# Kernel optimization log

Hardware: AMD Instinct MI355X
Metric: run time of the kernel (lower is better)

The kernel has to match this reference:

```python
import jax, jax.numpy as jnp
import numpy as np

N_NODES = 100000
N_EDGES = 1600000
HIDDEN = 128


def setup_inputs() -> dict:
    key = jax.random.key(0)
    k_x, k_w1, k_w2, k_v, k_i, k_o = jax.random.split(key, 6)
    x = jax.random.normal(k_x, (N_NODES, HIDDEN), dtype=jnp.float32)
    # gate1/gate2 are Linear(hidden,1,bias=False); store their weight rows as vectors
    w1 = jax.random.normal(k_w1, (HIDDEN,), dtype=jnp.float32) * 0.1
    w2 = jax.random.normal(k_w2, (HIDDEN,), dtype=jnp.float32) * 0.1
    adj_vals = jax.random.uniform(k_v, (N_EDGES,), dtype=jnp.float32)
    in_idx = jax.random.randint(k_i, (N_EDGES,), 0, N_NODES, dtype=jnp.int32)
    out_idx = jax.random.randint(k_o, (N_EDGES,), 0, N_NODES, dtype=jnp.int32)
    return {"x": x, "w1": w1, "w2": w2, "adj_vals": adj_vals,
            "in_idx": in_idx, "out_idx": out_idx}


def reference(x, w1, w2, adj_vals, in_idx, out_idx):
    # per-node gate scalars: x1 = gate1(x), x2 = gate2(x)  -> [N]
    x1 = x @ w1
    x2 = x @ w2
    # edge gate: tanh(x1[src] + x2[dst]) * adj_value  (dropout is identity in eval mode)
    m = jnp.tanh(x1[in_idx] + x2[out_idx]) * adj_vals  # [E]
    # sparse.mm(adj_alpha, x): out[i] = sum_{e: row(e)=i} m_e * x[col(e)]
    messages = m[:, None] * x[out_idx]                 # [E, d]
    result = jax.ops.segment_sum(messages, in_idx, num_segments=N_NODES)
    return result
```

## Files before the change

### kernel.cpp

```cpp
#include <hip/hip_runtime.h>

#define N_NODES 100000
#define N_EDGES 1600000
#define HIDDEN  128

#define NPB_SHIFT 9
#define NPB       512
#define NB        ((N_NODES + NPB - 1) / NPB)
#define PART_T    512
#define PART_EPT  16
#define PART_EPB  (PART_T * PART_EPT)
#define PART_B    ((N_EDGES + PART_EPB - 1) / PART_EPB)
#define HIST_EPT  16
#define HIST_EPB  (256 * HIST_EPT)
#define HIST_B    ((N_EDGES + HIST_EPB - 1) / HIST_EPB)
#define GATES_B   ((N_NODES * 32 + 255) / 256)
#define FINE_PE   20

#define SCAN_C 16
#define SCAN_T ((N_NODES + SCAN_C - 1) / SCAN_C)
#define SCAN_THREADS 6400
#define SCAN_B (SCAN_THREADS / 256)

__device__ __forceinline__ ushort f2bf(float f) {
    unsigned int u = __float_as_uint(f);
    u = (u + 0x7FFFu + ((u >> 16) & 1u)) >> 16;
    return (ushort)u;
}

__global__ void fagcn_zero(int* __restrict__ bcnt) {
    const int t = (int)threadIdx.x;
    if (t < NB) bcnt[t] = 0;
}

__global__ void fagcn_gates_hist(const float* __restrict__ x,
                                 const float* __restrict__ w1,
                                 const float* __restrict__ w2,
                                 const int*   __restrict__ in_idx,
                                 float* __restrict__ g1,
                                 float* __restrict__ g2,
                                 int*   __restrict__ bcnt,
                                 ushort* __restrict__ xh,
                                 int write_xh,
                                 int with_hist) {
    __shared__ int cnt[NB];
    if ((int)blockIdx.x < GATES_B) {
        const int tid  = blockIdx.x * 256 + (int)threadIdx.x;
        const int node = tid >> 5;
        const int hl   = (int)(threadIdx.x & 31);
        if (node >= N_NODES) return;

        const float4 xv  = *reinterpret_cast<const float4*>(x  + (size_t)node * HIDDEN + hl * 4);
        const float4 w1v = *reinterpret_cast<const float4*>(w1 + hl * 4);
        const float4 w2v = *reinterpret_cast<const float4*>(w2 + hl * 4);

        if (write_xh) {
            ushort4 h;
            h.x = f2bf(xv.x); h.y = f2bf(xv.y); h.z = f2bf(xv.z); h.w = f2bf(xv.w);
            *reinterpret_cast<ushort4*>(xh + (size_t)node * HIDDEN + hl * 4) = h;
        }

        float s1 = xv.x * w1v.x + xv.y * w1v.y + xv.z * w1v.z + xv.w * w1v.w;
        float s2 = xv.x * w2v.x + xv.y * w2v.y + xv.z * w2v.z + xv.w * w2v.w;

        #pragma unroll
        for (int off = 16; off > 0; off >>= 1) {
            s1 += __shfl_down(s1, off, 32);
            s2 += __shfl_down(s2, off, 32);
        }
        if (hl == 0) { g1[node] = s1; g2[node] = s2; }
    } else if (with_hist) {
        const int tid  = (int)threadIdx.x;
        const int base = ((int)blockIdx.x - GATES_B) * HIST_EPB + tid * HIST_EPT;
        for (int j = tid; j < NB; j += 256) cnt[j] = 0;
        __syncthreads();
        if (base < N_EDGES) {
            #pragma unroll
            for (int i = 0; i < 4; ++i) {
                const int4 v = *reinterpret_cast<const int4*>(in_idx + base + i * 4);
                atomicAdd(&cnt[v.x >> NPB_SHIFT], 1);
                atomicAdd(&cnt[v.y >> NPB_SHIFT], 1);
                atomicAdd(&cnt[v.z >> NPB_SHIFT], 1);
                atomicAdd(&cnt[v.w >> NPB_SHIFT], 1);
            }
        }
        __syncthreads();
        for (int j = tid; j < NB; j += 256)
            if (cnt[j]) atomicAdd(&bcnt[j], cnt[j]);
    }
}

__global__ void fagcn_scanb(const int* __restrict__ bcnt,
                            int* __restrict__ sbase,
                            int* __restrict__ bcur) {
    __shared__ int l[256];
    const int t = (int)threadIdx.x;
    const int c = (t < NB) ? bcnt[t] : 0;
    l[t] = c;
    __syncthreads();
    for (int off = 1; off < 256; off <<= 1) {
        int v = (t >= off) ? l[t - off] : 0;
        __syncthreads();
        l[t] += v;
        __syncthreads();
    }
    if (t < NB) { sbase[t] = l[t] - c; bcur[t] = 0; }
    if (t == NB - 1) sbase[NB] = l[t];
}

__global__ void fagcn_part(const float* __restrict__ adj,
                           const int*   __restrict__ in_idx,
                           const int*   __restrict__ out_idx,
                           const int*   __restrict__ sbase,
                           int*         __restrict__ bcur,
                           int2*        __restrict__ stage) {
    __shared__ int cnt[NB], lbase[NB], lcur[NB];
    const int tid  = (int)threadIdx.x;
    const int base = blockIdx.x * PART_EPB + tid * PART_EPT;

    for (int j = tid; j < NB; j += PART_T) { cnt[j] = 0; lcur[j] = 0; }
    __syncthreads();

    int s[PART_EPT];
    const bool act = (base < N_EDGES);
    if (act) {
        #pragma unroll
        for (int i = 0; i < PART_EPT / 4; ++i) {
            const int4 v = *reinterpret_cast<const int4*>(in_idx + base + i * 4);
            s[4 * i + 0] = v.x; s[4 * i + 1] = v.y;
            s[4 * i + 2] = v.z; s[4 * i + 3] = v.w;
        }
        #pragma unroll
        for (int i = 0; i < PART_EPT; ++i)
            atomicAdd(&cnt[s[i] >> NPB_SHIFT], 1);
    }
    __syncthreads();
    for (int j = tid; j < NB; j += PART_T)
        if (cnt[j] > 0) lbase[j] = sbase[j] + atomicAdd(&bcur[j], cnt[j]);
    __syncthreads();
    if (act) {
        #pragma unroll
        for (int i = 0; i < PART_EPT / 4; ++i) {
            const int4   d4 = *reinterpret_cast<const int4*>(out_idx + base + i * 4);
            const float4 a4 = *reinterpret_cast<const float4*>(adj + base + i * 4);
            const int   dd[4] = {d4.x, d4.y, d4.z, d4.w};
            const float aa[4] = {a4.x, a4.y, a4.z, a4.w};
            #pragma unroll
            for (int k = 0; k < 4; ++k) {
                const int src = s[4 * i + k];
                const int b   = src >> NPB_SHIFT;
                const int pos = lbase[b] + atomicAdd(&lcur[b], 1);
                stage[pos] = make_int2(((src & (NPB - 1)) << 17) | dd[k],
                                       __float_as_int(aa[k]));
            }
        }
    }
}

__global__ void fagcn_fine(const int2* __restrict__ stage,
                           const int*  __restrict__ sbase,
                           const float* __restrict__ g1,
                           const float* __restrict__ g2,
                           int*        __restrict__ offsets,
                           int2*       __restrict__ sedge) {
    __shared__ int cnt[NPB];
    __shared__ int cur[NPB];
    __shared__ float g1s[NPB];
    const int b = (int)blockIdx.x;
    const int t = (int)threadIdx.x;

    const int ebeg = sbase[b];
    const int eend = sbase[b + 1];
    const int node = (b << NPB_SHIFT) + t;

    g1s[t] = (node < N_NODES) ? g1[node] : 0.f;
    cnt[t] = 0;
    __syncthreads();

    int2  pay[FINE_PE];
    float gv[FINE_PE];
    #pragma unroll
    for (int i = 0; i < FINE_PE; ++i) {
        const int e = ebeg + t + i * NPB;
        if (e < eend) {
            pay[i] = stage[e];
            gv[i]  = g2[pay[i].x & 0x1FFFF];
            atomicAdd(&cnt[(unsigned)pay[i].x >> 17], 1);
        }
    }
    __syncthreads();

    const int c = cnt[t];
    for (int off = 1; off < NPB; off <<= 1) {
        int v = (t >= off) ? cnt[t - off] : 0;
        __syncthreads();
        cnt[t] += v;
        __syncthreads();
    }
    const int excl = cnt[t] - c;
    cur[t] = ebeg + excl;
    if (node < N_NODES) offsets[node] = ebeg + excl;
    if (b == (int)gridDim.x - 1 && t == 0) offsets[N_NODES] = N_EDGES;
    __syncthreads();

    #pragma unroll
    for (int i = 0; i < FINE_PE; ++i) {
        const int e = ebeg + t + i * NPB;
        if (e < eend) {
            const int slocal = (unsigned)pay[i].x >> 17;
            const float m = tanhf(g1s[slocal] + gv[i]) * __int_as_float(pay[i].y);
            const int pos = atomicAdd(&cur[slocal], 1);
            sedge[pos] = make_int2(pay[i].x & 0x1FFFF, __float_as_int(m));
        }
    }
}

__device__ __forceinline__ void acc8(float* a, uint4 v, float m) {
    const unsigned int u[4] = {v.x, v.y, v.z, v.w};
    #pragma unroll
    for (int i = 0; i < 4; ++i) {
        const float lo = __uint_as_float(u[i] << 16);
        const float hi = __uint_as_float(u[i] & 0xFFFF0000u);
        a[2 * i]     += m * lo;
        a[2 * i + 1] += m * hi;
    }
}

__global__ void fagcn_gather_bf16(const ushort* __restrict__ xh,
                                  const int*   __restrict__ offsets,
                                  const int2*  __restrict__ sedge,
                                  float*       __restrict__ out,
                                  int node_beg, int node_end) {
    const int wave = node_beg + (int)((blockIdx.x * blockDim.x + threadIdx.x) >> 6);
    const int lane = (int)(threadIdx.x & 63);
    if (wave >= node_end) return;

    const int beg = offsets[wave];
    const int end = offsets[wave + 1];
    const int q   = lane >> 4;
    const int ql  = lane & 15;

    float a[8] = {0.f, 0.f, 0.f, 0.f, 0.f, 0.f, 0.f, 0.f};
    float b[8] = {0.f, 0.f, 0.f, 0.f, 0.f, 0.f, 0.f, 0.f};

    int e = beg + q;
    for (; e + 12 < end; e += 16) {
        const int2 ed0 = sedge[e];
        const int2 ed1 = sedge[e + 4];
        const int2 ed2 = sedge[e + 8];
        const int2 ed3 = sedge[e + 12];
        const uint4 v0 = *reinterpret_cast<const uint4*>(xh + (size_t)ed0.x * HIDDEN + ql * 8);
        const uint4 v1 = *reinterpret_cast<const uint4*>(xh + (size_t)ed1.x * HIDDEN + ql * 8);
        const uint4 v2 = *reinterpret_cast<const uint4*>(xh + (size_t)ed2.x * HIDDEN + ql * 8);
        const uint4 v3 = *reinterpret_cast<const uint4*>(xh + (size_t)ed3.x * HIDDEN + ql * 8);
        acc8(a, v0, __int_as_float(ed0.y));
        acc8(b, v1, __int_as_float(ed1.y));
        acc8(a, v2, __int_as_float(ed2.y));
        acc8(b, v3, __int_as_float(ed3.y));
    }
    for (; e < end; e += 4) {
        const int2 ed = sedge[e];
        const uint4 v = *reinterpret_cast<const uint4*>(xh + (size_t)ed.x * HIDDEN + ql * 8);
        acc8(a, v, __int_as_float(ed.y));
    }

    float r[8];
    #pragma unroll
    for (int i = 0; i < 8; ++i) r[i] = a[i] + b[i];
    #pragma unroll
    for (int i = 0; i < 8; ++i) r[i] += __shfl(r[i], lane ^ 16, 64);
    #pragma unroll
    for (int i = 0; i < 8; ++i) r[i] += __shfl(r[i], lane ^ 32, 64);

    if (lane < 16) {
        float* o = out + (size_t)wave * HIDDEN + ql * 8;
        float4 lo = {r[0], r[1], r[2], r[3]};
        float4 hi = {r[4], r[5], r[6], r[7]};
        *reinterpret_cast<float4*>(o)     = lo;
        *reinterpret_cast<float4*>(o + 4) = hi;
    }
}

__global__ void fagcn_hist(const int* __restrict__ in_idx,
                           int* __restrict__ counts) {
    const int e = blockIdx.x * blockDim.x + threadIdx.x;
    if (e < N_EDGES) atomicAdd(&counts[in_idx[e]], 1);
}

__global__ void fagcn_zero_nodes(int* __restrict__ counts) {
    const int i = blockIdx.x * blockDim.x + threadIdx.x;
    if (i < N_NODES) counts[i] = 0;
}

__global__ void fagcn_scan1(const int* __restrict__ counts,
                            int* __restrict__ tsum) {
    const int t = blockIdx.x * blockDim.x + threadIdx.x;
    if (t >= SCAN_THREADS) return;
    int s = 0;
    if (t < SCAN_T) {
        const int beg = t * SCAN_C;
        const int end = (beg + SCAN_C < N_NODES) ? beg + SCAN_C : N_NODES;
        for (int i = beg; i < end; ++i) s += counts[i];
    }
    tsum[t] = s;
}

__global__ void fagcn_scan2(int* __restrict__ tsum) {
    __shared__ int lsum[1024];
    const int t = (int)threadIdx.x;
    const int C = (SCAN_THREADS + 1023) / 1024;
    const int beg = t * C;
    const int end = (beg + C < SCAN_THREADS) ? beg + C : SCAN_THREADS;
    int s = 0;
    for (int i = beg; i < end; ++i) s += tsum[i];
    lsum[t] = s;
    __syncthreads();
    for (int off = 1; off < 1024; off <<= 1) {
        int v = (t >= off) ? lsum[t - off] : 0;
        __syncthreads();
        lsum[t] += v;
        __syncthreads();
    }
    int prefix = (t == 0) ? 0 : lsum[t - 1];
    for (int i = beg; i < end; ++i) {
        const int v = tsum[i];
        tsum[i] = prefix;
        prefix += v;
    }
}

__global__ void fagcn_scan3(int* counts,
                            const int* __restrict__ tsum,
                            int* __restrict__ offsets) {
    const int t = blockIdx.x * blockDim.x + threadIdx.x;
    if (t >= SCAN_T) return;
    const int beg = t * SCAN_C;
    const int end = (beg + SCAN_C < N_NODES) ? beg + SCAN_C : N_NODES;
    int prefix = tsum[t];
    for (int i = beg; i < end; ++i) {
        const int c = counts[i];
        offsets[i] = prefix;
        prefix += c;
        counts[i] = 0;
    }
    if (t == 0) offsets[N_NODES] = N_EDGES;
}

__global__ void fagcn_bin(const float* __restrict__ adj,
                          const int*   __restrict__ in_idx,
                          const int*   __restrict__ out_idx,
                          const float* __restrict__ g1,
                          const float* __restrict__ g2,
                          const int*   __restrict__ offsets,
                          int*         __restrict__ cursor,
                          int2*        __restrict__ sedge) {
    const int e = blockIdx.x * blockDim.x + threadIdx.x;
    if (e >= N_EDGES) return;
    const int src = in_idx[e];
    const int dst = out_idx[e];
    const float m = tanhf(g1[src] + g2[dst]) * adj[e];
    const int pos = offsets[src] + atomicAdd(&cursor[src], 1);
    sedge[pos] = make_int2(dst, __float_as_int(m));
}

__global__ void fagcn_gather_f32(const float* __restrict__ x,
                                 const int*   __restrict__ offsets,
                                 const int2*  __restrict__ sedge,
                                 float*       __restrict__ out) {
    const int wave = (int)((blockIdx.x * blockDim.x + threadIdx.x) >> 6);
    const int lane = (int)(threadIdx.x & 63);
    if (wave >= N_NODES) return;
    const int beg  = offsets[wave];
    const int end  = offsets[wave + 1];
    const int half = lane >> 5;
    const int hl   = lane & 31;
    float4 a0 = {0.f, 0.f, 0.f, 0.f};
    float4 a1 = {0.f, 0.f, 0.f, 0.f};
    int e = beg + half;
    for (; e + 2 < end; e += 4) {
        const int2 ed0 = sedge[e];
        const int2 ed1 = sedge[e + 2];
        const float m0 = __int_as_float(ed0.y);
        const float m1 = __int_as_float(ed1.y);
        const float4 v0 = *reinterpret_cast<const float4*>(x + (size_t)ed0.x * HIDDEN + hl * 4);
        const float4 v1 = *reinterpret_cast<const float4*>(x + (size_t)ed1.x * HIDDEN + hl * 4);
        a0.x += m0 * v0.x; a0.y += m0 * v0.y; a0.z += m0 * v0.z; a0.w += m0 * v0.w;
        a1.x += m1 * v1.x; a1.y += m1 * v1.y; a1.z += m1 * v1.z; a1.w += m1 * v1.w;
    }
    for (; e < end; e += 2) {
        const int2 ed = sedge[e];
        const float m = __int_as_float(ed.y);
        const float4 v = *reinterpret_cast<const float4*>(x + (size_t)ed.x * HIDDEN + hl * 4);
        a0.x += m * v.x; a0.y += m * v.y; a0.z += m * v.z; a0.w += m * v.w;
    }
    float4 a;
    a.x = a0.x + a1.x; a.y = a0.y + a1.y; a.z = a0.z + a1.z; a.w = a0.w + a1.w;
    a.x += __shfl(a.x, lane ^ 32, 64);
    a.y += __shfl(a.y, lane ^ 32, 64);
    a.z += __shfl(a.z, lane ^ 32, 64);
    a.w += __shfl(a.w, lane ^ 32, 64);
    if (half == 0) {
        *reinterpret_cast<float4*>(out + (size_t)wave * HIDDEN + hl * 4) = a;
    }
}

extern "C" void kernel_launch(void* const* d_in, const int* in_sizes, int n_in,
                              void* d_out, int out_size, void* d_ws, size_t ws_size,
                              hipStream_t stream) {
    const float* x        = (const float*)d_in[0];
    const float* w1       = (const float*)d_in[1];
    const float* w2       = (const float*)d_in[2];
    const float* adj_vals = (const float*)d_in[3];
    const int*   in_idx   = (const int*)d_in[4];
    const int*   out_idx  = (const int*)d_in[5];
    float* out = (float*)d_out;

    ushort* xh      = (ushort*)d_ws;
    int2*   sedge   = (int2*)(xh + (size_t)N_NODES * HIDDEN);
    int2*   stage   = sedge + N_EDGES;
    float*  g1      = (float*)(stage + N_EDGES);
    float*  g2      = g1 + N_NODES;
    int*    offsets = (int*)(g2 + N_NODES);
    int*    cursor  = offsets + N_NODES + 1;
    int*    tsum    = cursor + N_NODES;
    int*    bcnt    = tsum + SCAN_THREADS;
    int*    sbase   = bcnt + NB;
    int*    bcur    = sbase + NB + 1;

    const size_t need_full = (size_t)((char*)(bcur + NB) - (char*)d_ws);
    const size_t need_old  = need_full - (size_t)N_EDGES * 8;
    const int full_path = (ws_size >= need_full);
    const int bf16_ok   = (ws_size >= need_old);

    if (full_path) {
        fagcn_zero<<<1, 256, 0, stream>>>(bcnt);
        fagcn_gates_hist<<<GATES_B + HIST_B, 256, 0, stream>>>(
            x, w1, w2, in_idx, g1, g2, bcnt, xh, 1, 1);
        fagcn_scanb<<<1, 256, 0, stream>>>(bcnt, sbase, bcur);
        fagcn_part<<<PART_B, PART_T, 0, stream>>>(
            adj_vals, in_idx, out_idx, sbase, bcur, stage);
        fagcn_fine<<<NB, NPB, 0, stream>>>(
            stage, sbase, g1, g2, offsets, sedge);
        const int half_nodes = N_NODES / 2;
        fagcn_gather_bf16<<<(half_nodes + 3) / 4, 256, 0, stream>>>(
            xh, offsets, sedge, out, 0, half_nodes);
        fagcn_gather_bf16<<<(N_NODES - half_nodes + 3) / 4, 256, 0, stream>>>(
            xh, offsets, sedge, out, half_nodes, N_NODES);
    } else {
        if (!bf16_ok) sedge = (int2*)d_ws;
        fagcn_gates_hist<<<GATES_B, 256, 0, stream>>>(
            x, w1, w2, in_idx, g1, g2, bcnt, xh, bf16_ok, 0);
        fagcn_zero_nodes<<<(N_NODES + 255) / 256, 256, 0, stream>>>(cursor);
        fagcn_hist<<<(N_EDGES + 255) / 256, 256, 0, stream>>>(in_idx, cursor);
        fagcn_scan1<<<SCAN_B, 256, 0, stream>>>(cursor, tsum);
        fagcn_scan2<<<1, 1024, 0, stream>>>(tsum);
        fagcn_scan3<<<SCAN_B, 256, 0, stream>>>(cursor, tsum, offsets);
        fagcn_bin<<<(N_EDGES + 255) / 256, 256, 0, stream>>>(
            adj_vals, in_idx, out_idx, g1, g2, offsets, cursor, sedge);
        if (bf16_ok) {
            fagcn_gather_bf16<<<(N_NODES + 3) / 4, 256, 0, stream>>>(
                xh, offsets, sedge, out, 0, N_NODES);
        } else {
            fagcn_gather_f32<<<(N_NODES + 3) / 4, 256, 0, stream>>>(
                x, offsets, sedge, out);
        }
    }
}
```

Before: 149.9 us.

## Reuse atomic ranks for scatter, wave-shuffle scan in fine pass, merge gather launches

The partition and fine-bin kernels now keep the return value of the counting atomicAdd as each edge's rank within its bucket. That removes the second pass of shared-memory atomics used to assign write positions. The fine kernel's 512-element block scan, which needed a __syncthreads per step, becomes a wave-level shuffle scan followed by a small per-wave prefix. The two half-size gather launches are merged into one, and the partition kernel moves to 1024 threads with 8 edges each. Output order inside a bucket may differ, which can change floating-point summation order slightly.

After: 144.0 us. -4.0%, faster.

```diff
diff --git a/kernel.cpp b/kernel.cpp
--- a/kernel.cpp
+++ b/kernel.cpp
@@ -7,8 +7,8 @@
 #define NPB_SHIFT 9
 #define NPB       512
 #define NB        ((N_NODES + NPB - 1) / NPB)
-#define PART_T    512
-#define PART_EPT  16
+#define PART_T    1024
+#define PART_EPT  8
 #define PART_EPB  (PART_T * PART_EPT)
 #define PART_B    ((N_EDGES + PART_EPB - 1) / PART_EPB)
 #define HIST_EPT  16
@@ -114,14 +114,14 @@
                            const int*   __restrict__ sbase,
                            int*         __restrict__ bcur,
                            int2*        __restrict__ stage) {
-    __shared__ int cnt[NB], lbase[NB], lcur[NB];
+    __shared__ int cnt[NB], lbase[NB];
     const int tid  = (int)threadIdx.x;
     const int base = blockIdx.x * PART_EPB + tid * PART_EPT;
 
-    for (int j = tid; j < NB; j += PART_T) { cnt[j] = 0; lcur[j] = 0; }
-    __syncthreads();
-
-    int s[PART_EPT];
+    for (int j = tid; j < NB; j += PART_T) cnt[j] = 0;
+    __syncthreads();
+
+    int s[PART_EPT], rank[PART_EPT];
     const bool act = (base < N_EDGES);
     if (act) {
         #pragma unroll
@@ -132,7 +132,7 @@
         }
         #pragma unroll
         for (int i = 0; i < PART_EPT; ++i)
-            atomicAdd(&cnt[s[i] >> NPB_SHIFT], 1);
+            rank[i] = atomicAdd(&cnt[s[i] >> NPB_SHIFT], 1);
     }
     __syncthreads();
     for (int j = tid; j < NB; j += PART_T)
@@ -147,11 +147,12 @@
             const float aa[4] = {a4.x, a4.y, a4.z, a4.w};
             #pragma unroll
             for (int k = 0; k < 4; ++k) {
-                const int src = s[4 * i + k];
+                const int e   = 4 * i + k;
+                const int src = s[e];
                 const int b   = src >> NPB_SHIFT;
-                const int pos = lbase[b] + atomicAdd(&lcur[b], 1);
-                stage[pos] = make_int2(((src & (NPB - 1)) << 17) | dd[k],
-                                       __float_as_int(aa[k]));
+                stage[lbase[b] + rank[e]] =
+                    make_int2(((src & (NPB - 1)) << 17) | dd[k],
+                              __float_as_int(aa[k]));
             }
         }
     }
@@ -163,11 +164,14 @@
                            const float* __restrict__ g2,
                            int*        __restrict__ offsets,
                            int2*       __restrict__ sedge) {
-    __shared__ int cnt[NPB];
-    __shared__ int cur[NPB];
+    __shared__ int   cnt[NPB];
+    __shared__ int   nbase[NPB];
+    __shared__ int   wsum[NPB / 64];
     __shared__ float g1s[NPB];
-    const int b = (int)blockIdx.x;
-    const int t = (int)threadIdx.x;
+    const int b    = (int)blockIdx.x;
+    const int t    = (int)threadIdx.x;
+    const int w    = t >> 6;
+    const int lane = t & 63;
 
     const int ebeg = sbase[b];
     const int eend = sbase[b + 1];
@@ -179,26 +183,39 @@
 
     int2  pay[FINE_PE];
     float gv[FINE_PE];
+    int   rank[FINE_PE];
     #pragma unroll
     for (int i = 0; i < FINE_PE; ++i) {
         const int e = ebeg + t + i * NPB;
         if (e < eend) {
-            pay[i] = stage[e];
-            gv[i]  = g2[pay[i].x & 0x1FFFF];
-            atomicAdd(&cnt[(unsigned)pay[i].x >> 17], 1);
+            pay[i]  = stage[e];
+            gv[i]   = g2[pay[i].x & 0x1FFFF];
+            rank[i] = atomicAdd(&cnt[(unsigned)pay[i].x >> 17], 1);
         }
     }
     __syncthreads();
 
     const int c = cnt[t];
-    for (int off = 1; off < NPB; off <<= 1) {
-        int v = (t >= off) ? cnt[t - off] : 0;
-        __syncthreads();
-        cnt[t] += v;
-        __syncthreads();
-    }
-    const int excl = cnt[t] - c;
-    cur[t] = ebeg + excl;
+    int v = c;
+    #pragma unroll
+    for (int off = 1; off < 64; off <<= 1) {
+        const int u = __shfl_up(v, off, 64);
+        if (lane >= off) v += u;
+    }
+    if (lane == 63) wsum[w] = v;
+    __syncthreads();
+    if (t == 0) {
+        int acc = 0;
+        #pragma unroll
+        for (int j = 0; j < NPB / 64; ++j) {
+            const int xw = wsum[j];
+            wsum[j] = acc;
+            acc += xw;
+        }
+    }
+    __syncthreads();
+    const int excl = v - c + wsum[w];
+    nbase[t] = ebeg + excl;
     if (node < N_NODES) offsets[node] = ebeg + excl;
     if (b == (int)gridDim.x - 1 && t == 0) offsets[N_NODES] = N_EDGES;
     __syncthreads();
@@ -209,8 +226,8 @@
         if (e < eend) {
             const int slocal = (unsigned)pay[i].x >> 17;
             const float m = tanhf(g1s[slocal] + gv[i]) * __int_as_float(pay[i].y);
-            const int pos = atomicAdd(&cur[slocal], 1);
-            sedge[pos] = make_int2(pay[i].x & 0x1FFFF, __float_as_int(m));
+            sedge[nbase[slocal] + rank[i]] =
+                make_int2(pay[i].x & 0x1FFFF, __float_as_int(m));
         }
     }
 }
@@ -229,11 +246,10 @@
 __global__ void fagcn_gather_bf16(const ushort* __restrict__ xh,
                                   const int*   __restrict__ offsets,
                                   const int2*  __restrict__ sedge,
-                                  float*       __restrict__ out,
-                                  int node_beg, int node_end) {
-    const int wave = node_beg + (int)((blockIdx.x * blockDim.x + threadIdx.x) >> 6);
+                                  float*       __restrict__ out) {
+    const int wave = (int)((blockIdx.x * blockDim.x + threadIdx.x) >> 6);
     const int lane = (int)(threadIdx.x & 63);
-    if (wave >= node_end) return;
+    if (wave >= N_NODES) return;
 
     const int beg = offsets[wave];
     const int end = offsets[wave + 1];
@@ -441,11 +457,8 @@
             adj_vals, in_idx, out_idx, sbase, bcur, stage);
         fagcn_fine<<<NB, NPB, 0, stream>>>(
             stage, sbase, g1, g2, offsets, sedge);
-        const int half_nodes = N_NODES / 2;
-        fagcn_gather_bf16<<<(half_nodes + 3) / 4, 256, 0, stream>>>(
-            xh, offsets, sedge, out, 0, half_nodes);
-        fagcn_gather_bf16<<<(N_NODES - half_nodes + 3) / 4, 256, 0, stream>>>(
-            xh, offsets, sedge, out, half_nodes, N_NODES);
+        fagcn_gather_bf16<<<(N_NODES + 3) / 4, 256, 0, stream>>>(
+            xh, offsets, sedge, out);
     } else {
         if (!bf16_ok) sedge = (int2*)d_ws;
         fagcn_gates_hist<<<GATES_B, 256, 0, stream>>>(
@@ -459,7 +472,7 @@
             adj_vals, in_idx, out_idx, g1, g2, offsets, cursor, sedge);
         if (bf16_ok) {
             fagcn_gather_bf16<<<(N_NODES + 3) / 4, 256, 0, stream>>>(
-                xh, offsets, sedge, out, 0, N_NODES);
+                xh, offsets, sedge, out);
         } else {
             fagcn_gather_f32<<<(N_NODES + 3) / 4, 256, 0, stream>>>(
                 x, offsets, sedge, out);
```
